# Kernel tuning notes

Hardware: AMD Instinct MI355X
Metric: run time of the kernel (lower is better)

The kernel has to match this reference:

```python
import jax, jax.numpy as jnp
import numpy as np

NUM_CLASSES = 21
THRESHOLD = 0.5
VAR0, VAR1 = 0.1, 0.2
NEGPOS_RATIO = 3


def setup_inputs() -> dict:
    key = jax.random.key(0)
    k1, k2, k3, k4, k5, k6, k7 = jax.random.split(key, 7)
    B, P, C, O = 64, 8732, 21, 8
    loc_data = jax.random.normal(k1, (B, P, 4), dtype=jnp.float32) * 0.1
    conf_data = jax.random.normal(k2, (B, P, C), dtype=jnp.float32)
    # priors: center form (cx, cy, w, h), valid in [0,1]
    cxy = jax.random.uniform(k3, (P, 2), minval=0.05, maxval=0.95)
    pwh = jax.random.uniform(k4, (P, 2), minval=0.05, maxval=0.3)
    priors = jnp.concatenate([cxy, pwh], axis=-1).astype(jnp.float32)
    # targets: corner-form boxes + class label (float), (B, O, 5)
    tc = jax.random.uniform(k5, (B, O, 2), minval=0.2, maxval=0.8)
    twh = jax.random.uniform(k6, (B, O, 2), minval=0.1, maxval=0.4)
    tmin = jnp.clip(tc - twh / 2, 0.0, 1.0)
    tmax = jnp.clip(tc + twh / 2, 0.0, 1.0)
    labels = jax.random.randint(k7, (B, O, 1), 0, C - 1).astype(jnp.float32)
    targets = jnp.concatenate([tmin, tmax, labels], axis=-1)
    return {"loc_data": loc_data, "conf_data": conf_data, "priors": priors, "targets": targets}


def _point_form(p):
    # (cx,cy,w,h) -> (xmin,ymin,xmax,ymax)
    return jnp.concatenate([p[:, :2] - p[:, 2:] / 2, p[:, :2] + p[:, 2:] / 2], axis=-1)


def _jaccard(a, b):
    # a: (O,4) corners, b: (P,4) corners -> (O,P)
    lt = jnp.maximum(a[:, None, :2], b[None, :, :2])
    rb = jnp.minimum(a[:, None, 2:], b[None, :, 2:])
    wh = jnp.clip(rb - lt, 0.0, None)
    inter = wh[..., 0] * wh[..., 1]
    area_a = ((a[:, 2] - a[:, 0]) * (a[:, 3] - a[:, 1]))[:, None]
    area_b = ((b[:, 2] - b[:, 0]) * (b[:, 3] - b[:, 1]))[None, :]
    return inter / (area_a + area_b - inter)


def _match_one(truths, labels, priors_pt, priors):
    # truths: (O,4) corners, labels: (O,), priors: (P,4) center-form
    ov = _jaccard(truths, priors_pt)                      # (O,P)
    best_prior_idx = jnp.argmax(ov, axis=1)               # (O,)
    best_truth_overlap = jnp.max(ov, axis=0)              # (P,)
    best_truth_idx = jnp.argmax(ov, axis=0)               # (P,)
    # ensure every gt box matches its best prior
    best_truth_overlap = best_truth_overlap.at[best_prior_idx].set(2.0)
    best_truth_idx = best_truth_idx.at[best_prior_idx].set(jnp.arange(truths.shape[0]))
    matched = truths[best_truth_idx]                      # (P,4)
    conf = labels[best_truth_idx].astype(jnp.int32) + 1
    conf = jnp.where(best_truth_overlap < THRESHOLD, 0, conf)
    # encode offsets
    g_cxcy = ((matched[:, :2] + matched[:, 2:]) / 2 - priors[:, :2]) / (VAR0 * priors[:, 2:])
    g_wh = jnp.log(jnp.clip((matched[:, 2:] - matched[:, :2]) / priors[:, 2:], 1e-8, None)) / VAR1
    return jnp.concatenate([g_cxcy, g_wh], axis=-1), conf


def _forward(loc_data, conf_data, priors, targets):
    B, P, C = conf_data.shape
    priors_sg = jax.lax.stop_gradient(priors)             # torch uses .data
    targets_sg = jax.lax.stop_gradient(targets)
    priors_pt = _point_form(priors_sg)
    loc_t, conf_t = jax.vmap(_match_one, in_axes=(0, 0, None, None))(
        targets_sg[:, :, :4], targets_sg[:, :, 4], priors_pt, priors_sg)
    pos = conf_t > 0                                      # (B,P)

    # localization: smooth L1 summed over positive priors
    diff = loc_data - loc_t
    ad = jnp.abs(diff)
    sl1 = jnp.where(ad < 1.0, 0.5 * diff * diff, ad - 0.5)
    loss_l = jnp.sum(sl1 * pos[..., None].astype(sl1.dtype))

    # per-prior conf loss for hard negative mining
    lse = jax.nn.logsumexp(conf_data, axis=-1)            # (B,P)
    gathered = jnp.take_along_axis(conf_data, conf_t[..., None], axis=-1)[..., 0]
    loss_c_all = lse - gathered                           # (B,P)
    mined = jnp.where(pos, 0.0, loss_c_all)
    loss_idx = jnp.argsort(-mined, axis=1)                # descending
    idx_rank = jnp.argsort(loss_idx, axis=1)
    num_pos = jnp.sum(pos.astype(jnp.int32), axis=1, keepdims=True)  # (B,1)
    num_neg = jnp.minimum(NEGPOS_RATIO * num_pos, P - num_pos)
    neg = idx_rank < num_neg                              # (B,P)

    sel = (pos | neg).astype(loss_c_all.dtype)
    loss_c = jnp.sum(loss_c_all * sel)

    N = jnp.sum(num_pos).astype(loss_l.dtype)
    return loss_l / N, loss_c / N


def reference(loc_data, conf_data, priors, targets):
    return _forward(loc_data, conf_data, priors, targets)
```

## Files before the change

kernel.cpp:

```cpp
#include <hip/hip_runtime.h>
#include <math.h>

#define TPB 256
#define TPBS 1024
#define LDSF 12288

typedef unsigned long long ull;
typedef float pf4 __attribute__((ext_vector_type(4), aligned(4)));

__device__ __forceinline__ float jac(float tx0, float ty0, float tx1, float ty1, float ta,
                                     float px0, float py0, float px1, float py1, float pa) {
    float ltx = fmaxf(tx0, px0), lty = fmaxf(ty0, py0);
    float rbx = fminf(tx1, px1), rby = fminf(ty1, py1);
    float w = fmaxf(rbx - ltx, 0.0f), h = fmaxf(rby - lty, 0.0f);
    float inter = w * h;
    return inter / (ta + pa - inter);
}

template <int ON, int CN>
__global__ __launch_bounds__(TPB) void fused_kernel(
    const float* __restrict__ loc, const float* __restrict__ priors,
    const float* __restrict__ targets, const float* __restrict__ conf,
    int P, int O_rt, int C_rt, int CB2,
    float* __restrict__ mined, ull* __restrict__ pkeys,
    float* __restrict__ part_ll, float* __restrict__ part_pc,
    int* __restrict__ part_np) {
    constexpr int OMAX = (ON > 0) ? ON : 64;
    constexpr int CC = (CN > 0) ? CN : 32;
    const int O = (ON > 0) ? ON : O_rt;
    const int C = (CN > 0) ? CN : C_rt;
    const int b = blockIdx.x / CB2;
    const int chunk = blockIdx.x % CB2;
    const int tid = threadIdx.x;
    const int p = chunk * TPB + tid;
    const bool pv = (p < P);
    const int lane = tid & 63, wv = tid >> 6;

    __shared__ float s_tx0[OMAX], s_ty0[OMAX], s_tx1[OMAX], s_ty1[OMAX];
    __shared__ float s_lab[OMAX], s_area[OMAX];
    __shared__ ull s_wk[TPB / 64][OMAX];
    __shared__ float s_wll[TPB / 64], s_wpc[TPB / 64];
    __shared__ int s_wnp[TPB / 64];

    float rv[CC];
    float4 pr4 = make_float4(0.f, 0.f, 1.f, 1.f);
    if (pv) {
        const float* row = conf + ((size_t)b * P + p) * C;
        if (CN > 0) {
#pragma unroll
            for (int q = 0; q < CN / 4; ++q) {
                pf4 v = *(const pf4*)(row + 4 * q);
#pragma unroll
                for (int e = 0; e < 4; ++e) rv[4 * q + e] = v[e];
            }
#pragma unroll
            for (int j = (CN / 4) * 4; j < CN; ++j) rv[j] = row[j];
        } else {
            for (int j = 0; j < C; ++j) rv[j] = row[j];
        }
        pr4 = ((const float4*)priors)[p];
    }

    for (int o = tid; o < O; o += TPB) {
        const float* t = targets + ((size_t)b * O + o) * 5;
        float x0 = t[0], y0 = t[1], x1 = t[2], y1 = t[3];
        s_tx0[o] = x0; s_ty0[o] = y0; s_tx1[o] = x1; s_ty1[o] = y1;
        s_lab[o] = t[4];
        s_area[o] = (x1 - x0) * (y1 - y0);
    }
    __syncthreads();

    float cx = pr4.x, cy = pr4.y, pw = pr4.z, ph = pr4.w;
    float px0 = cx - pw * 0.5f, py0 = cy - ph * 0.5f;
    float px1 = cx + pw * 0.5f, py1 = cy + ph * 0.5f;
    float pa = (px1 - px0) * (py1 - py0);
    float bto = -1.0f;
    int bti = 0;
    for (int o = 0; o < O; ++o) {
        ull kk = 0ull;
        if (pv) {
            float ov = jac(s_tx0[o], s_ty0[o], s_tx1[o], s_ty1[o], s_area[o],
                           px0, py0, px1, py1, pa);
            kk = ((ull)__float_as_uint(ov) << 32) |
                 (ull)(0xFFFFFFFFu - (unsigned)p);
            if (ov > bto) { bto = ov; bti = o; }
        }
#pragma unroll
        for (int d = 1; d < 64; d <<= 1) {
            ull other = __shfl_xor(kk, d, 64);
            if (other > kk) kk = other;
        }
        if (lane == 0) s_wk[wv][o] = kk;
    }
    __syncthreads();
    if (tid < O) {
        ull kk = s_wk[0][tid];
        for (int w = 1; w < TPB / 64; ++w)
            if (s_wk[w][tid] > kk) kk = s_wk[w][tid];
        pkeys[((size_t)b * O + tid) * CB2 + chunk] = kk;
    }

    float ll = 0.0f, pc = 0.0f;
    int np = 0;
    if (pv) {
        float m = rv[0];
#pragma unroll
        for (int j = 1; j < CC; ++j) { if (CN > 0 || j < C) m = fmaxf(m, rv[j]); }
        float s = 0.0f;
#pragma unroll
        for (int j = 0; j < CC; ++j) { if (CN > 0 || j < C) s += expf(rv[j] - m); }
        float lse = m + logf(s);

        int c = (bto < 0.5f) ? 0 : ((int)s_lab[bti] + 1);
        float rowc = rv[0];
#pragma unroll
        for (int j = 1; j < CC; ++j) { if (CN > 0 || j < C) { if (c == j) rowc = rv[j]; } }
        float lc = lse - rowc;

        bool pos = c > 0;
        mined[(size_t)b * P + p] = pos ? 0.0f : lc;
        if (pos) {
            pc = lc;
            np = 1;
            float mx0 = s_tx0[bti], my0 = s_ty0[bti];
            float mx1 = s_tx1[bti], my1 = s_ty1[bti];
            float g0 = ((mx0 + mx1) * 0.5f - cx) / (0.1f * pw);
            float g1 = ((my0 + my1) * 0.5f - cy) / (0.1f * ph);
            float g2 = logf(fmaxf((mx1 - mx0) / pw, 1e-8f)) / 0.2f;
            float g3 = logf(fmaxf((my1 - my0) / ph, 1e-8f)) / 0.2f;
            float4 ld = ((const float4*)loc)[(size_t)b * P + p];
            float gt4[4] = {g0, g1, g2, g3};
            float lv[4] = {ld.x, ld.y, ld.z, ld.w};
#pragma unroll
            for (int q = 0; q < 4; ++q) {
                float d = lv[q] - gt4[q];
                float ad = fabsf(d);
                ll += (ad < 1.0f) ? 0.5f * d * d : (ad - 0.5f);
            }
        }
    }

#pragma unroll
    for (int d = 1; d < 64; d <<= 1) {
        ll += __shfl_xor(ll, d, 64);
        pc += __shfl_xor(pc, d, 64);
        np += __shfl_xor(np, d, 64);
    }
    if (lane == 0) { s_wll[wv] = ll; s_wpc[wv] = pc; s_wnp[wv] = np; }
    __syncthreads();
    if (tid == 0) {
        float L = 0.f, Pc = 0.f;
        int N = 0;
        for (int w = 0; w < TPB / 64; ++w) { L += s_wll[w]; Pc += s_wpc[w]; N += s_wnp[w]; }
        part_ll[blockIdx.x] = L;
        part_pc[blockIdx.x] = Pc;
        part_np[blockIdx.x] = N;
    }
}

template <int ON, int CN>
__global__ __launch_bounds__(TPBS) void select_kernel(
    const float* __restrict__ mined, const float* __restrict__ conf,
    const float* __restrict__ loc, const float* __restrict__ priors,
    const float* __restrict__ targets, const ull* __restrict__ pkeys,
    const float* __restrict__ part_ll, const float* __restrict__ part_pc,
    const int* __restrict__ part_np,
    float* __restrict__ ll_batch, float* __restrict__ lc_batch,
    int* __restrict__ np_batch,
    int P, int O_rt, int C_rt, int CB2, int ratio) {
    constexpr int OMAX = (ON > 0) ? ON : 64;
    const int O = (ON > 0) ? ON : O_rt;
    const int C = (CN > 0) ? CN : C_rt;
    const int b = blockIdx.x, tid = threadIdx.x;
    const int lane = tid & 63, wv = tid >> 6;
    constexpr int W = TPBS / 64;
    const float* v = mined + (size_t)b * P;
    const bool lds = (P <= LDSF);

    __shared__ float s_m[LDSF];
    __shared__ int s_hist[W * 256];
    __shared__ float s_tx0[OMAX], s_ty0[OMAX], s_tx1[OMAX], s_ty1[OMAX];
    __shared__ float s_lab[OMAX], s_area[OMAX];
    __shared__ ull s_keys[OMAX];
    __shared__ int s_bp[OMAX];
    __shared__ float s_wf[W], s_wg[W];
    __shared__ int s_wi[W];
    __shared__ int s_wt[4];
    __shared__ unsigned s_bsel;
    __shared__ int s_krn;
    __shared__ float s_bc[2], s_fix[2];
    __shared__ int s_bn, s_fixn;

    if (lds) {
        for (int i = tid; i < P; i += TPBS) s_m[i] = v[i];
    }
    float pll = 0.0f, ppc = 0.0f;
    int pnp = 0;
    for (int i = tid; i < CB2; i += TPBS) {
        pll += part_ll[b * CB2 + i];
        ppc += part_pc[b * CB2 + i];
        pnp += part_np[b * CB2 + i];
    }
#pragma unroll
    for (int d = 1; d < 64; d <<= 1) {
        pll += __shfl_xor(pll, d, 64);
        ppc += __shfl_xor(ppc, d, 64);
        pnp += __shfl_xor(pnp, d, 64);
    }
    if (lane == 0) { s_wf[wv] = pll; s_wg[wv] = ppc; s_wi[wv] = pnp; }

    if (tid < O) {
        const float* t = targets + ((size_t)b * O + tid) * 5;
        float x0 = t[0], y0 = t[1], x1 = t[2], y1 = t[3];
        s_tx0[tid] = x0; s_ty0[tid] = y0; s_tx1[tid] = x1; s_ty1[tid] = y1;
        s_lab[tid] = t[4];
        s_area[tid] = (x1 - x0) * (y1 - y0);
        s_keys[tid] = 0ull;
    }
    __syncthreads();

    for (int i = tid; i < O * CB2; i += TPBS) {
        int o = i / CB2, s = i % CB2;
        atomicMax(&s_keys[o], pkeys[((size_t)b * O + o) * CB2 + s]);
    }
    __syncthreads();
    if (tid < O)
        s_bp[tid] = (int)(0xFFFFFFFFu - (unsigned)(s_keys[tid] & 0xFFFFFFFFull));
    __syncthreads();

    if (lds && tid < O) s_m[s_bp[tid]] = 0.0f;

    float dll = 0.0f, dpc = 0.0f;
    int dnp = 0;
    if (tid < O) {
        const int o = tid;
        const int p = s_bp[o];
        bool owner = true;
        for (int o2 = o + 1; o2 < O; ++o2)
            if (s_bp[o2] == p) owner = false;
        if (owner) {
            float4 pr = ((const float4*)priors)[p];
            float cx = pr.x, cy = pr.y, pw = pr.z, ph = pr.w;
            float px0 = cx - pw * 0.5f, py0 = cy - ph * 0.5f;
            float px1 = cx + pw * 0.5f, py1 = cy + ph * 0.5f;
            float pa = (px1 - px0) * (py1 - py0);
            float bto = -1.0f;
            int bti = 0;
            for (int o2 = 0; o2 < O; ++o2) {
                float ov = jac(s_tx0[o2], s_ty0[o2], s_tx1[o2], s_ty1[o2], s_area[o2],
                               px0, py0, px1, py1, pa);
                if (ov > bto) { bto = ov; bti = o2; }
            }
            int c_t = (bto < 0.5f) ? 0 : ((int)s_lab[bti] + 1);
            const float* row = conf + ((size_t)b * P + p) * C;
            float m = row[0];
            for (int j = 1; j < C; ++j) m = fmaxf(m, row[j]);
            float s = 0.0f;
            for (int j = 0; j < C; ++j) s += expf(row[j] - m);
            float lse = m + logf(s);
            int c_n = (int)s_lab[o] + 1;
            float lc_n = lse - row[c_n];
            bool pos_t = c_t > 0;
            float lc_t = lse - row[c_t];
            dpc = lc_n - (pos_t ? lc_t : 0.0f);
            dnp = 1 - (pos_t ? 1 : 0);
            float4 ld = ((const float4*)loc)[(size_t)b * P + p];
            float lv[4] = {ld.x, ld.y, ld.z, ld.w};
            float sl_new = 0.0f, sl_old = 0.0f;
            {
                float mx0 = s_tx0[o], my0 = s_ty0[o], mx1 = s_tx1[o], my1 = s_ty1[o];
                float g[4] = {((mx0 + mx1) * 0.5f - cx) / (0.1f * pw),
                              ((my0 + my1) * 0.5f - cy) / (0.1f * ph),
                              logf(fmaxf((mx1 - mx0) / pw, 1e-8f)) / 0.2f,
                              logf(fmaxf((my1 - my0) / ph, 1e-8f)) / 0.2f};
                for (int q = 0; q < 4; ++q) {
                    float d = lv[q] - g[q];
                    float ad = fabsf(d);
                    sl_new += (ad < 1.0f) ? 0.5f * d * d : (ad - 0.5f);
                }
            }
            if (pos_t) {
                float mx0 = s_tx0[bti], my0 = s_ty0[bti], mx1 = s_tx1[bti], my1 = s_ty1[bti];
                float g[4] = {((mx0 + mx1) * 0.5f - cx) / (0.1f * pw),
                              ((my0 + my1) * 0.5f - cy) / (0.1f * ph),
                              logf(fmaxf((mx1 - mx0) / pw, 1e-8f)) / 0.2f,
                              logf(fmaxf((my1 - my0) / ph, 1e-8f)) / 0.2f};
                for (int q = 0; q < 4; ++q) {
                    float d = lv[q] - g[q];
                    float ad = fabsf(d);
                    sl_old += (ad < 1.0f) ? 0.5f * d * d : (ad - 0.5f);
                }
            }
            dll = sl_new - sl_old;
        }
    }
    if (wv == 0) {
#pragma unroll
        for (int d = 1; d < 64; d <<= 1) {
            dll += __shfl_xor(dll, d, 64);
            dpc += __shfl_xor(dpc, d, 64);
            dnp += __shfl_xor(dnp, d, 64);
        }
        if (lane == 0) { s_fix[0] = dll; s_fix[1] = dpc; s_fixn = dnp; }
    }
    __syncthreads();
    if (tid == 0) {
        float L = 0.f, Pc = 0.f;
        int N = 0;
        for (int w = 0; w < W; ++w) { L += s_wf[w]; Pc += s_wg[w]; N += s_wi[w]; }
        s_bc[0] = L + s_fix[0]; s_bc[1] = Pc + s_fix[1]; s_bn = N + s_fixn;
    }
    __syncthreads();
    const float ll_sum = s_bc[0];
    const float sum_pos = s_bc[1];
    const int npos = s_bn;

    const int k = min(ratio * npos, P - npos);
    if (tid == 0) {
        ll_batch[b] = ll_sum;
        np_batch[b] = npos;
    }
    if (k <= 0) {
        if (tid == 0) lc_batch[b] = sum_pos;
        return;
    }

    unsigned prefix = 0u;
    int kr = k;
    for (int pass = 0; pass < 4; ++pass) {
        const int shift = 24 - 8 * pass;
        const unsigned mask = (pass == 0) ? 0u : (0xFFFFFFFFu << (32 - 8 * pass));
        for (int i = tid; i < W * 256; i += TPBS) s_hist[i] = 0;
        __syncthreads();
        for (int i = tid; i < P; i += TPBS) {
            float x;
            if (lds) x = s_m[i];
            else {
                x = v[i];
                for (int o = 0; o < O; ++o)
                    if (i == s_bp[o]) x = 0.0f;
            }
            unsigned u = __float_as_uint(x);
            if ((u & mask) == prefix)
                atomicAdd(&s_hist[wv * 256 + ((u >> shift) & 0xFF)], 1);
        }
        __syncthreads();
        int sge = 0, h = 0;
        if (tid < 256) {
            for (int w = 0; w < W; ++w) h += s_hist[w * 256 + tid];
            int val = h;
#pragma unroll
            for (int d = 1; d < 64; d <<= 1) {
                int t = __shfl_down(val, d, 64);
                if (lane + d < 64) val += t;
            }
            if (lane == 0) s_wt[tid >> 6] = val;
            sge = val;
        }
        __syncthreads();
        if (tid < 256) {
            for (int w = (tid >> 6) + 1; w < 4; ++w) sge += s_wt[w];
            int sgt = sge - h;
            if (sge >= kr && sgt < kr) {
                s_bsel = (unsigned)tid;
                s_krn = kr - sgt;
            }
        }
        __syncthreads();
        prefix |= s_bsel << shift;
        kr = s_krn;
    }
    const float T = __uint_as_float(prefix);
    float lsum = 0.0f;
    int lcnt = 0;
    for (int i = tid; i < P; i += TPBS) {
        float x;
        if (lds) x = s_m[i];
        else {
            x = v[i];
            for (int o = 0; o < O; ++o)
                if (i == s_bp[o]) x = 0.0f;
        }
        if (x > T) { lsum += x; ++lcnt; }
    }
#pragma unroll
    for (int d = 1; d < 64; d <<= 1) {
        lsum += __shfl_xor(lsum, d, 64);
        lcnt += __shfl_xor(lcnt, d, 64);
    }
    if (lane == 0) { s_wf[wv] = lsum; s_wi[wv] = lcnt; }
    __syncthreads();
    if (tid == 0) {
        float S = 0.f;
        int Cn = 0;
        for (int w = 0; w < W; ++w) { S += s_wf[w]; Cn += s_wi[w]; }
        lc_batch[b] = sum_pos + S + (float)(k - Cn) * T;
    }
}

__global__ __launch_bounds__(TPB) void finalize_kernel(
    const float* __restrict__ ll_batch, const int* __restrict__ np_batch,
    const float* __restrict__ lc_batch, int B, float* __restrict__ out) {
    const int tid = threadIdx.x;
    __shared__ float s_l[TPB], s_c[TPB];
    __shared__ int s_n[TPB];
    float l = 0.0f, c = 0.0f;
    int n = 0;
    for (int i = tid; i < B; i += TPB) {
        l += ll_batch[i];
        c += lc_batch[i];
        n += np_batch[i];
    }
    s_l[tid] = l; s_c[tid] = c; s_n[tid] = n;
    __syncthreads();
    for (int s = TPB / 2; s > 0; s >>= 1) {
        if (tid < s) {
            s_l[tid] += s_l[tid + s];
            s_c[tid] += s_c[tid + s];
            s_n[tid] += s_n[tid + s];
        }
        __syncthreads();
    }
    if (tid == 0) {
        float N = (float)s_n[0];
        out[0] = s_l[0] / N;
        out[1] = s_c[0] / N;
    }
}

extern "C" void kernel_launch(void* const* d_in, const int* in_sizes, int n_in,
                              void* d_out, int out_size, void* d_ws, size_t ws_size,
                              hipStream_t stream) {
    const float* loc = (const float*)d_in[0];
    const float* conf = (const float*)d_in[1];
    const float* priors = (const float*)d_in[2];
    const float* targets = (const float*)d_in[3];

    const int P = in_sizes[2] / 4;
    const int B = in_sizes[0] / (P * 4);
    const int C = in_sizes[1] / (in_sizes[0] / 4);
    const int O = in_sizes[3] / (B * 5);
    const size_t BP = (size_t)B * P;
    const int CB2 = (P + TPB - 1) / TPB;

    ull* pkeys = (ull*)d_ws;
    float* mined = (float*)(pkeys + (size_t)B * O * CB2);
    float* part_ll = mined + BP;
    float* part_pc = part_ll + (size_t)B * CB2;
    int* part_np = (int*)(part_pc + (size_t)B * CB2);
    float* ll_batch = (float*)(part_np + (size_t)B * CB2);
    float* lc_batch = ll_batch + B;
    int* np_batch = (int*)(lc_batch + B);

    if (O == 8 && C == 21) {
        fused_kernel<8, 21><<<B * CB2, TPB, 0, stream>>>(
            loc, priors, targets, conf, P, O, C, CB2,
            mined, pkeys, part_ll, part_pc, part_np);
        select_kernel<8, 21><<<B, TPBS, 0, stream>>>(
            mined, conf, loc, priors, targets, pkeys, part_ll, part_pc, part_np,
            ll_batch, lc_batch, np_batch, P, O, C, CB2, 3);
    } else {
        fused_kernel<0, 0><<<B * CB2, TPB, 0, stream>>>(
            loc, priors, targets, conf, P, O, C, CB2,
            mined, pkeys, part_ll, part_pc, part_np);
        select_kernel<0, 0><<<B, TPBS, 0, stream>>>(
            mined, conf, loc, priors, targets, pkeys, part_ll, part_pc, part_np,
            ll_batch, lc_batch, np_batch, P, O, C, CB2, 3);
    }

    finalize_kernel<<<1, TPB, 0, stream>>>(ll_batch, np_batch, lc_batch, B,
                                           (float*)d_out);
}
```

Measured before the change: 125.3 us.

## Use float shuffle max with ballot, fast math, and aggregated radix histogram

Replaces the 64-bit key shuffle reduction in the per-truth best-prior search with a 32-bit float max reduction, then uses a ballot to pick the lowest matching lane and build the key. The conf log-sum-exp now uses the fast __expf/__logf intrinsics. The radix-select histogram changes to a bin-major padded layout (stride 17), and the first pass aggregates equal bins across the wavefront with a ballot loop so fewer contended LDS atomics are issued. Fast intrinsics may change results slightly, and the ballot loop adds serial iterations when bins are diverse.

```diff
diff --git a/kernel.cpp b/kernel.cpp
--- a/kernel.cpp
+++ b/kernel.cpp
@@ -4,6 +4,7 @@
 #define TPB 256
 #define TPBS 1024
 #define LDSF 12288
+#define HP 17
 
 typedef unsigned long long ull;
 typedef float pf4 __attribute__((ext_vector_type(4), aligned(4)));
@@ -77,18 +78,22 @@
     float bto = -1.0f;
     int bti = 0;
     for (int o = 0; o < O; ++o) {
+        float ov = -1.0f;
+        if (pv) {
+            ov = jac(s_tx0[o], s_ty0[o], s_tx1[o], s_ty1[o], s_area[o],
+                     px0, py0, px1, py1, pa);
+            if (ov > bto) { bto = ov; bti = o; }
+        }
+        float mx = ov;
+#pragma unroll
+        for (int d = 1; d < 64; d <<= 1)
+            mx = fmaxf(mx, __shfl_xor(mx, d, 64));
         ull kk = 0ull;
-        if (pv) {
-            float ov = jac(s_tx0[o], s_ty0[o], s_tx1[o], s_ty1[o], s_area[o],
-                           px0, py0, px1, py1, pa);
-            kk = ((ull)__float_as_uint(ov) << 32) |
-                 (ull)(0xFFFFFFFFu - (unsigned)p);
-            if (ov > bto) { bto = ov; bti = o; }
-        }
-#pragma unroll
-        for (int d = 1; d < 64; d <<= 1) {
-            ull other = __shfl_xor(kk, d, 64);
-            if (other > kk) kk = other;
+        if (mx >= 0.0f) {
+            ull msk = __ballot(ov == mx);
+            int src = __ffsll(msk) - 1;
+            unsigned pw_ = (unsigned)(chunk * TPB + (wv << 6) + src);
+            kk = ((ull)__float_as_uint(mx) << 32) | (ull)(0xFFFFFFFFu - pw_);
         }
         if (lane == 0) s_wk[wv][o] = kk;
     }
@@ -108,8 +113,8 @@
         for (int j = 1; j < CC; ++j) { if (CN > 0 || j < C) m = fmaxf(m, rv[j]); }
         float s = 0.0f;
 #pragma unroll
-        for (int j = 0; j < CC; ++j) { if (CN > 0 || j < C) s += expf(rv[j] - m); }
-        float lse = m + logf(s);
+        for (int j = 0; j < CC; ++j) { if (CN > 0 || j < C) s += __expf(rv[j] - m); }
+        float lse = m + __logf(s);
 
         int c = (bto < 0.5f) ? 0 : ((int)s_lab[bti] + 1);
         float rowc = rv[0];
@@ -178,7 +183,7 @@
     const bool lds = (P <= LDSF);
 
     __shared__ float s_m[LDSF];
-    __shared__ int s_hist[W * 256];
+    __shared__ int s_hist[256 * HP];
     __shared__ float s_tx0[OMAX], s_ty0[OMAX], s_tx1[OMAX], s_ty1[OMAX];
     __shared__ float s_lab[OMAX], s_area[OMAX];
     __shared__ ull s_keys[OMAX];
@@ -256,8 +261,8 @@
             float m = row[0];
             for (int j = 1; j < C; ++j) m = fmaxf(m, row[j]);
             float s = 0.0f;
-            for (int j = 0; j < C; ++j) s += expf(row[j] - m);
-            float lse = m + logf(s);
+            for (int j = 0; j < C; ++j) s += __expf(row[j] - m);
+            float lse = m + __logf(s);
             int c_n = (int)s_lab[o] + 1;
             float lc_n = lse - row[c_n];
             bool pos_t = c_t > 0;
@@ -330,7 +335,7 @@
     for (int pass = 0; pass < 4; ++pass) {
         const int shift = 24 - 8 * pass;
         const unsigned mask = (pass == 0) ? 0u : (0xFFFFFFFFu << (32 - 8 * pass));
-        for (int i = tid; i < W * 256; i += TPBS) s_hist[i] = 0;
+        for (int i = tid; i < 256 * HP; i += TPBS) s_hist[i] = 0;
         __syncthreads();
         for (int i = tid; i < P; i += TPBS) {
             float x;
@@ -341,13 +346,26 @@
                     if (i == s_bp[o]) x = 0.0f;
             }
             unsigned u = __float_as_uint(x);
-            if ((u & mask) == prefix)
-                atomicAdd(&s_hist[wv * 256 + ((u >> shift) & 0xFF)], 1);
+            bool match = ((u & mask) == prefix);
+            int bin = (u >> shift) & 0xFF;
+            if (pass == 0) {
+                ull act = __ballot(match);
+                while (act) {
+                    int src = __ffsll(act) - 1;
+                    int b0 = __shfl(bin, src, 64);
+                    ull same = __ballot(match && bin == b0) & act;
+                    if (lane == src)
+                        atomicAdd(&s_hist[b0 * HP + wv], (int)__popcll(same));
+                    act &= ~same;
+                }
+            } else if (match) {
+                atomicAdd(&s_hist[bin * HP + wv], 1);
+            }
         }
         __syncthreads();
         int sge = 0, h = 0;
         if (tid < 256) {
-            for (int w = 0; w < W; ++w) h += s_hist[w * 256 + tid];
+            for (int w = 0; w < W; ++w) h += s_hist[tid * HP + w];
             int val = h;
 #pragma unroll
             for (int d = 1; d < 64; d <<= 1) {
```

New measurement: 121.1 us. 3.3% less time.
